# Optimization experiments

Hardware: AMD Instinct MI355X
Metric: run time of the kernel (lower is better)

The kernel has to match this reference:

```python
import jax, jax.numpy as jnp
import numpy as np

NEG = -10000.0
SLOPE = 0.2


def setup_inputs() -> dict:
    key = jax.random.key(0)
    k1, k2, k3, k4, k5 = jax.random.split(key, 5)
    B, N, F_in, F_out = 8, 2048, 512, 512
    text = jax.random.normal(k1, (B, N, F_in), dtype=jnp.float32)
    adj = jax.random.randint(k2, (B, N, N), 0, 2, dtype=jnp.int32)
    sc = 1.0 / np.sqrt(F_in)
    W = jax.random.normal(k3, (F_in, F_out), dtype=jnp.float32) * sc
    b = jnp.zeros((F_out,), dtype=jnp.float32)
    a_src = jax.random.normal(k4, (F_out,), dtype=jnp.float32) * sc
    a_dst = jax.random.normal(k5, (F_out,), dtype=jnp.float32) * sc
    return {"text": text, "adj": adj, "W": W, "b": b, "a_src": a_src, "a_dst": a_dst}


def reference(text, adj, W, b, a_src, a_dst):
    # hidden: [B, N, F_out]
    hidden = jnp.einsum("bnf,fo->bno", text, W) + b
    s = jnp.einsum("bno,o->bn", hidden, a_src)  # src score per node
    d = jnp.einsum("bno,o->bn", hidden, a_dst)  # dst score per node
    scores = s[:, :, None] + d[:, None, :]      # [B, N, N]
    scores = jnp.where(scores >= 0, scores, SLOPE * scores)  # LeakyReLU
    # faithful to original: masked_fill where adj.bool() is True
    scores = jnp.where(adj.astype(bool), NEG, scores)
    attn = jax.nn.softmax(scores, axis=-1)
    return jnp.einsum("bnm,bmo->bno", attn, hidden)
```

## Files before the change

### kernel.cpp

```cpp
#include <hip/hip_runtime.h>
#include <stdint.h>

#define NB 8
#define NN 2048
#define NF 512
#define TOTN (NB * NN)

typedef unsigned short u16;
typedef short bf16x8 __attribute__((ext_vector_type(8)));
typedef float f32x4 __attribute__((ext_vector_type(4)));

__device__ __forceinline__ u16 f2bf(float x) {
  unsigned u = __float_as_uint(x);
  unsigned r = 0x7FFFu + ((u >> 16) & 1u);
  return (u16)((u + r) >> 16);
}

__device__ __forceinline__ void gl2lds16(const void* g, void* l) {
  __builtin_amdgcn_global_load_lds((const __attribute__((address_space(1))) void*)g,
                                   (__attribute__((address_space(3))) void*)l,
                                   16, 0, 0);
}


__global__ __launch_bounds__(256) void conv_kernel(
    const float* __restrict__ text, const float* __restrict__ W,
    u16* __restrict__ text_bf, u16* __restrict__ Wt) {
  int blk = blockIdx.x;
  if (blk < 8192) {
    int idx = blk * 256 + threadIdx.x;
    float4 v = ((const float4*)text)[idx];
    ushort4 o;
    o.x = f2bf(v.x); o.y = f2bf(v.y); o.z = f2bf(v.z); o.w = f2bf(v.w);
    ((ushort4*)text_bf)[idx] = o;
  } else {
    int t = (blk - 8192) * 256 + threadIdx.x;
    int o = t >> 9, f = t & 511;
    Wt[o * NF + f] = f2bf(W[f * NF + o]);
  }
}

__global__ __launch_bounds__(256) void pack_kernel(
    const int* __restrict__ adj, uint32_t* __restrict__ bm) {
  int bid = blockIdx.x;
  int z = bid & 7, idx = bid >> 3;
  int gid = z * 131072 + idx * 256 + threadIdx.x;
  const int4* p = (const int4*)(adj + (size_t)gid * 32);
  uint32_t bits = 0;
#pragma unroll
  for (int c = 0; c < 8; ++c) {
    int4 a = p[c];
    bits |= (uint32_t)(a.x != 0) << (c * 4 + 0);
    bits |= (uint32_t)(a.y != 0) << (c * 4 + 1);
    bits |= (uint32_t)(a.z != 0) << (c * 4 + 2);
    bits |= (uint32_t)(a.w != 0) << (c * 4 + 3);
  }
  bm[gid] = bits;
}

__global__ __launch_bounds__(256) void gemm1_kernel(
    const u16* __restrict__ A,
    const u16* __restrict__ Bt,
    const float* __restrict__ bias, const float* __restrict__ a_src,
    const float* __restrict__ a_dst, u16* __restrict__ Bg,
    float* __restrict__ s, float* __restrict__ d) {
  __shared__ u16 Alds[128 * 32];
  __shared__ u16 Blds[128 * 32];

  const int bid = blockIdx.x;
  const int zx = bid & 7, u = (bid >> 3) & 15, bm_ = bid >> 7;
  const int bn = zx * 16 + u;
  const int t = threadIdx.x, wave = t >> 6, lane = t & 63;
  const int wm = (wave >> 1) * 64, wn = (wave & 1) * 64;

  f32x4 acc[4][4];
#pragma unroll
  for (int i = 0; i < 4; ++i)
#pragma unroll
    for (int j = 0; j < 4; ++j) acc[i][j] = (f32x4){0.f, 0.f, 0.f, 0.f};

  const int rowA0 = bm_ * 128, rowB0 = bn * 128;
  const int srow = (lane >> 2);
  const int scol = (lane & 3) * 8;

  for (int kt = 0; kt < NF; kt += 32) {
#pragma unroll
    for (int q = 0; q < 2; ++q) {
      int r = wave * 32 + q * 16;
      gl2lds16(A + (size_t)(rowA0 + r + srow) * NF + (kt + scol), &Alds[r * 32]);
    }
#pragma unroll
    for (int q = 0; q < 2; ++q) {
      int r = wave * 32 + q * 16;
      gl2lds16(Bt + (size_t)(rowB0 + r + srow) * NF + (kt + scol), &Blds[r * 32]);
    }
    __syncthreads();

    const int fr = lane & 15;
    const int k0 = (lane >> 4) * 8;
    bf16x8 af[4], bfr[4];
#pragma unroll
    for (int i = 0; i < 4; ++i)
      af[i] = *(const bf16x8*)&Alds[(wm + i * 16 + fr) * 32 + k0];
#pragma unroll
    for (int j = 0; j < 4; ++j)
      bfr[j] = *(const bf16x8*)&Blds[(wn + j * 16 + fr) * 32 + k0];
#pragma unroll
    for (int i = 0; i < 4; ++i)
#pragma unroll
      for (int j = 0; j < 4; ++j)
        acc[i][j] = __builtin_amdgcn_mfma_f32_16x16x32_bf16(af[i], bfr[j],
                                                            acc[i][j], 0, 0, 0);
    __syncthreads();
  }

  const int quad = lane >> 4, ln16 = lane & 15;
  float sa[4] = {0.f, 0.f, 0.f, 0.f}, da[4] = {0.f, 0.f, 0.f, 0.f};
#pragma unroll
  for (int i = 0; i < 4; ++i) {
    int m0 = bm_ * 128 + wm + i * 16 + quad * 4;
#pragma unroll
    for (int r = 0; r < 4; ++r) {
      int m = m0 + r;
      float bv = bias[m];
      float asv = a_src[m], adv = a_dst[m];
      int oc = m >> 4, oln = m & 15;
#pragma unroll
      for (int j = 0; j < 4; ++j) {
        int n = bn * 128 + wn + j * 16 + ln16;
        float h = acc[i][j][r] + bv;
        int zz = n >> 11, nz = n & 2047;
        int kc = nz >> 5, kq = (nz >> 3) & 3, ke = nz & 7;
        size_t off = ((size_t)zz << 20) + (((size_t)kc * 32 + oc) << 9) +
                     ((kq * 16 + oln) << 3) + ke;
        Bg[off] = f2bf(h);
        sa[j] = fmaf(h, asv, sa[j]);
        da[j] = fmaf(h, adv, da[j]);
      }
    }
  }
#pragma unroll
  for (int j = 0; j < 4; ++j) {
    float v = sa[j] + __shfl_xor(sa[j], 16, 64);
    v += __shfl_xor(v, 32, 64);
    float w2 = da[j] + __shfl_xor(da[j], 16, 64);
    w2 += __shfl_xor(w2, 32, 64);
    if (quad == 0) {
      int n = bn * 128 + wn + j * 16 + ln16;
      atomicAdd(&s[n], v);
      atomicAdd(&d[n], w2);
    }
  }
}

__global__ __launch_bounds__(512, 2) void fused_attn_kernel(
    const uint32_t* __restrict__ bm, const float* __restrict__ s,
    const float* __restrict__ d, const u16* __restrict__ Bg,
    float* __restrict__ out) {
  __shared__ u16 Plds[2][4096];
  __shared__ float lpart[512];
  __shared__ float linv_lds[64];

  const int bid = blockIdx.x;
  const int z = bid & 7;
  const int i0 = (bid >> 3) * 64;
  const int t = threadIdx.x, wave = t >> 6, lane = t & 63;
  const int quad = lane >> 4, ln16 = lane & 15;

  const int pr = t >> 3;
  const int ko = (t & 7) * 8;
  const float si = s[z * NN + i0 + pr];
  const uint32_t* bmrow = bm + (size_t)(z * NN + i0 + pr) * 64;
  const float* db = d + z * NN;

  const u16* BgZ = Bg + ((size_t)z << 20);

  f32x4 acc[4][4];
#pragma unroll
  for (int i = 0; i < 4; ++i)
#pragma unroll
    for (int j = 0; j < 4; ++j) acc[i][j] = (f32x4){0.f, 0.f, 0.f, 0.f};

  uint32_t bw = bmrow[ko >> 5];
  float4 dv0 = *(const float4*)&db[ko];
  float4 dv1 = *(const float4*)&db[ko + 4];

  const int prc = pr & 15, pch = pr >> 4;
  const int ph = ko >> 5, pq = (ko >> 3) & 3;
  const int pwoff = ph * 2048 + pch * 512 +
                    (prc * 4 + (pq ^ ((prc >> 1) & 3))) * 8;
  const int fslot = ln16 * 4 + (quad ^ ((ln16 >> 1) & 3));

  float lsum = 0.f;
  int par = 0;

  for (int kt = 0; kt < NN; kt += 64, par ^= 1) {
    uint32_t bits8 = (bw >> (ko & 31)) & 0xFFu;
    float dva[8];
    *(float4*)&dva[0] = dv0;
    *(float4*)&dva[4] = dv1;
    u16 pk[8];
#pragma unroll
    for (int e = 0; e < 8; ++e) {
      float x = si + dva[e];
      float xm = fmaxf(x, 0.2f * x);
      float p = ((bits8 >> e) & 1u) ? 0.f : __expf(xm);
      lsum += p;
      pk[e] = f2bf(p);
    }
    *(int4*)((u16*)Plds + par * 4096 + pwoff) = *(int4*)pk;

    __syncthreads();

    const int kc0 = kt >> 5;
    bf16x8 bfr[2][4];
#pragma unroll
    for (int h = 0; h < 2; ++h)
#pragma unroll
      for (int j = 0; j < 4; ++j)
        bfr[h][j] = *(const bf16x8*)&BgZ[(((size_t)(kc0 + h) * 32 +
                                           (wave * 4 + j)) << 9) + lane * 8];

    if (kt + 64 < NN) {
      bw = bmrow[((kt + 64) >> 5) + (ko >> 5)];
      dv0 = *(const float4*)&db[kt + 64 + ko];
      dv1 = *(const float4*)&db[kt + 64 + ko + 4];
    }

    bf16x8 af[2][4];
#pragma unroll
    for (int h = 0; h < 2; ++h)
#pragma unroll
      for (int i = 0; i < 4; ++i)
        af[h][i] = *(const bf16x8*)((const u16*)Plds + par * 4096 + h * 2048 +
                                    i * 512 + fslot * 8);
#pragma unroll
    for (int h = 0; h < 2; ++h)
#pragma unroll
      for (int i = 0; i < 4; ++i)
#pragma unroll
        for (int j = 0; j < 4; ++j)
          acc[i][j] = __builtin_amdgcn_mfma_f32_16x16x32_bf16(af[h][i],
                                                              bfr[h][j],
                                                              acc[i][j], 0, 0, 0);
  }

  lpart[pr * 8 + (t & 7)] = lsum;
  __syncthreads();
  if (t < 64) {
    const float* lp = &lpart[t * 8];
    float tot = ((lp[0] + lp[1]) + (lp[2] + lp[3])) +
                ((lp[4] + lp[5]) + (lp[6] + lp[7]));
    linv_lds[t] = 1.0f / tot;
  }
  __syncthreads();

#pragma unroll
  for (int i = 0; i < 4; ++i) {
#pragma unroll
    for (int r = 0; r < 4; ++r) {
      int m = i * 16 + quad * 4 + r;
      float sc = linv_lds[m];
      float* ob = out + ((size_t)(z * NN) + i0 + m) * NF + wave * 64;
#pragma unroll
      for (int j = 0; j < 4; ++j) ob[j * 16 + ln16] = acc[i][j][r] * sc;
    }
  }
}

extern "C" void kernel_launch(void* const* d_in, const int* in_sizes, int n_in,
                              void* d_out, int out_size, void* d_ws,
                              size_t ws_size, hipStream_t stream) {
  const float* text  = (const float*)d_in[0];
  const int*   adj   = (const int*)d_in[1];
  const float* W     = (const float*)d_in[2];
  const float* bias  = (const float*)d_in[3];
  const float* a_src = (const float*)d_in[4];
  const float* a_dst = (const float*)d_in[5];
  float* out = (float*)d_out;

  char* ws = (char*)d_ws;
  u16*      text_bf = (u16*)(ws + 0);
  u16*      Wt      = (u16*)(ws + 16777216);
  u16*      Bg      = (u16*)(ws + 17301504);
  float*    s       = (float*)(ws + 34078720);
  float*    d       = (float*)(ws + 34144256);
  uint32_t* bmask   = (uint32_t*)(ws + 34209792);

  hipMemsetAsync(s, 0, 131072, stream);

  conv_kernel<<<9216, 256, 0, stream>>>(text, W, text_bf, Wt);
  pack_kernel<<<4096, 256, 0, stream>>>(adj, bmask);

  gemm1_kernel<<<512, 256, 0, stream>>>(Wt, text_bf, bias, a_src, a_dst, Bg, s, d);

  fused_attn_kernel<<<256, 512, 0, stream>>>(bmask, s, d, Bg, out);
}
```

Baseline: 303.5 us.

## Compute softmax probabilities in registers as MFMA A-fragments, drop LDS staging

The attention kernel now has each wave build its P fragments directly in registers in the MFMA A-operand layout, removing the shared-memory P buffer and its per-iteration barrier. To match, the adjacency bitmask is stored column-major and the hidden matrix layout is re-tiled into 128-wide output-feature slabs. Blocks now tile 256 rows by 128 output features with 256 threads, so the exp work is repeated across the four feature slabs. P also uses cheaper round-half-up bf16 conversion. The cost is 4x redundant exp/mask computation, more accumulator registers (4x8 tiles), and uncoalesced 4-byte bitmask reads.

```diff
diff --git a/kernel.cpp b/kernel.cpp
--- a/kernel.cpp
+++ b/kernel.cpp
@@ -14,6 +14,10 @@
   unsigned u = __float_as_uint(x);
   unsigned r = 0x7FFFu + ((u >> 16) & 1u);
   return (u16)((u + r) >> 16);
+}
+
+__device__ __forceinline__ float felem(float4 q, int e) {
+  return (e == 0) ? q.x : (e == 1) ? q.y : (e == 2) ? q.z : q.w;
 }
 
 __device__ __forceinline__ void gl2lds16(const void* g, void* l) {
@@ -41,11 +45,12 @@
 }
 
 __global__ __launch_bounds__(256) void pack_kernel(
-    const int* __restrict__ adj, uint32_t* __restrict__ bm) {
+    const int* __restrict__ adj, uint32_t* __restrict__ bmT) {
   int bid = blockIdx.x;
   int z = bid & 7, idx = bid >> 3;
-  int gid = z * 131072 + idx * 256 + threadIdx.x;
-  const int4* p = (const int4*)(adj + (size_t)gid * 32);
+  int widx = idx * 256 + threadIdx.x;
+  int row = widx >> 6, col = widx & 63;
+  const int4* p = (const int4*)(adj + ((size_t)z * 131072 + widx) * 32);
   uint32_t bits = 0;
 #pragma unroll
   for (int c = 0; c < 8; ++c) {
@@ -55,7 +60,7 @@
     bits |= (uint32_t)(a.z != 0) << (c * 4 + 2);
     bits |= (uint32_t)(a.w != 0) << (c * 4 + 3);
   }
-  bm[gid] = bits;
+  bmT[z * 131072 + col * 2048 + row] = bits;
 }
 
 __global__ __launch_bounds__(256) void gemm1_kernel(
@@ -124,14 +129,14 @@
       int m = m0 + r;
       float bv = bias[m];
       float asv = a_src[m], adv = a_dst[m];
-      int oc = m >> 4, oln = m & 15;
+      int otp = m >> 7, jf = (m >> 4) & 7, oln = m & 15;
 #pragma unroll
       for (int j = 0; j < 4; ++j) {
         int n = bn * 128 + wn + j * 16 + ln16;
         float h = acc[i][j][r] + bv;
         int zz = n >> 11, nz = n & 2047;
         int kc = nz >> 5, kq = (nz >> 3) & 3, ke = nz & 7;
-        size_t off = ((size_t)zz << 20) + (((size_t)kc * 32 + oc) << 9) +
+        size_t off = (((size_t)zz * 4 + otp) << 18) + (kc << 12) + (jf << 9) +
                      ((kq * 16 + oln) << 3) + ke;
         Bg[off] = f2bf(h);
         sa[j] = fmaf(h, asv, sa[j]);
@@ -153,117 +158,126 @@
   }
 }
 
-__global__ __launch_bounds__(512, 2) void fused_attn_kernel(
-    const uint32_t* __restrict__ bm, const float* __restrict__ s,
+__global__ __launch_bounds__(256, 1) void fused_attn_kernel(
+    const uint32_t* __restrict__ bmT, const float* __restrict__ s,
     const float* __restrict__ d, const u16* __restrict__ Bg,
     float* __restrict__ out) {
-  __shared__ u16 Plds[2][4096];
-  __shared__ float lpart[512];
-  __shared__ float linv_lds[64];
+  __shared__ float linv_lds[4][64];
 
   const int bid = blockIdx.x;
   const int z = bid & 7;
-  const int i0 = (bid >> 3) * 64;
+  const int rest = bid >> 3;
+  const int it = rest & 7, ot = rest >> 3;
   const int t = threadIdx.x, wave = t >> 6, lane = t & 63;
   const int quad = lane >> 4, ln16 = lane & 15;
-
-  const int pr = t >> 3;
-  const int ko = (t & 7) * 8;
-  const float si = s[z * NN + i0 + pr];
-  const uint32_t* bmrow = bm + (size_t)(z * NN + i0 + pr) * 64;
-  const float* db = d + z * NN;
-
-  const u16* BgZ = Bg + ((size_t)z << 20);
-
-  f32x4 acc[4][4];
-#pragma unroll
-  for (int i = 0; i < 4; ++i)
-#pragma unroll
-    for (int j = 0; j < 4; ++j) acc[i][j] = (f32x4){0.f, 0.f, 0.f, 0.f};
-
-  uint32_t bw = bmrow[ko >> 5];
-  float4 dv0 = *(const float4*)&db[ko];
-  float4 dv1 = *(const float4*)&db[ko + 4];
-
-  const int prc = pr & 15, pch = pr >> 4;
-  const int ph = ko >> 5, pq = (ko >> 3) & 3;
-  const int pwoff = ph * 2048 + pch * 512 +
-                    (prc * 4 + (pq ^ ((prc >> 1) & 3))) * 8;
-  const int fslot = ln16 * 4 + (quad ^ ((ln16 >> 1) & 3));
-
-  float lsum = 0.f;
-  int par = 0;
-
-  for (int kt = 0; kt < NN; kt += 64, par ^= 1) {
-    uint32_t bits8 = (bw >> (ko & 31)) & 0xFFu;
-    float dva[8];
-    *(float4*)&dva[0] = dv0;
-    *(float4*)&dva[4] = dv1;
-    u16 pk[8];
-#pragma unroll
-    for (int e = 0; e < 8; ++e) {
-      float x = si + dva[e];
-      float xm = fmaxf(x, 0.2f * x);
-      float p = ((bits8 >> e) & 1u) ? 0.f : __expf(xm);
-      lsum += p;
-      pk[e] = f2bf(p);
-    }
-    *(int4*)((u16*)Plds + par * 4096 + pwoff) = *(int4*)pk;
-
-    __syncthreads();
-
+  const int i0w = it * 256 + wave * 64;
+
+  const float* sz = s + z * NN;
+  const float* dz = d + z * NN;
+  const uint32_t* bmz = bmT + z * 131072;
+  const u16* BgW = Bg + (((size_t)z * 4 + ot) << 18);
+
+  float si[4];
+  int rowv[4];
+#pragma unroll
+  for (int f = 0; f < 4; ++f) {
+    rowv[f] = i0w + f * 16 + ln16;
+    si[f] = sz[rowv[f]];
+  }
+
+  f32x4 acc[4][8];
+#pragma unroll
+  for (int f = 0; f < 4; ++f)
+#pragma unroll
+    for (int j = 0; j < 8; ++j) acc[f][j] = (f32x4){0.f, 0.f, 0.f, 0.f};
+
+  float lsum[4] = {0.f, 0.f, 0.f, 0.f};
+
+  uint32_t wcur[4][2];
+  float4 dcur[4];
+#pragma unroll
+  for (int f = 0; f < 4; ++f) {
+    wcur[f][0] = bmz[0 * 2048 + rowv[f]];
+    wcur[f][1] = bmz[1 * 2048 + rowv[f]];
+  }
+#pragma unroll
+  for (int h = 0; h < 2; ++h)
+#pragma unroll
+    for (int c = 0; c < 2; ++c)
+      dcur[h * 2 + c] = *(const float4*)&dz[h * 32 + quad * 8 + c * 4];
+
+  for (int kt = 0; kt < NN; kt += 64) {
     const int kc0 = kt >> 5;
-    bf16x8 bfr[2][4];
+
+    bf16x8 bfr[2][8];
 #pragma unroll
     for (int h = 0; h < 2; ++h)
 #pragma unroll
-      for (int j = 0; j < 4; ++j)
-        bfr[h][j] = *(const bf16x8*)&BgZ[(((size_t)(kc0 + h) * 32 +
-                                           (wave * 4 + j)) << 9) + lane * 8];
+      for (int j = 0; j < 8; ++j)
+        bfr[h][j] = *(const bf16x8*)&BgW[(size_t)(kc0 + h) * 4096 + j * 512 +
+                                         lane * 8];
+
+    bf16x8 af[2][4];
+#pragma unroll
+    for (int f = 0; f < 4; ++f) {
+#pragma unroll
+      for (int h = 0; h < 2; ++h) {
+        uint32_t bits = wcur[f][h] >> (quad * 8);
+#pragma unroll
+        for (int e = 0; e < 8; ++e) {
+          float dj = felem(dcur[h * 2 + (e >> 2)], e & 3);
+          float x = si[f] + dj;
+          float xm = fmaxf(x, 0.2f * x);
+          float p = ((bits >> e) & 1u) ? 0.f : __expf(xm);
+          lsum[f] += p;
+          af[h][f][e] = (short)((__float_as_uint(p) + 0x8000u) >> 16);
+        }
+      }
+    }
 
     if (kt + 64 < NN) {
-      bw = bmrow[((kt + 64) >> 5) + (ko >> 5)];
-      dv0 = *(const float4*)&db[kt + 64 + ko];
-      dv1 = *(const float4*)&db[kt + 64 + ko + 4];
-    }
-
-    bf16x8 af[2][4];
+      int c0 = (kt + 64) >> 5;
+#pragma unroll
+      for (int f = 0; f < 4; ++f) {
+        wcur[f][0] = bmz[(c0 + 0) * 2048 + rowv[f]];
+        wcur[f][1] = bmz[(c0 + 1) * 2048 + rowv[f]];
+      }
+#pragma unroll
+      for (int h = 0; h < 2; ++h)
+#pragma unroll
+        for (int c = 0; c < 2; ++c)
+          dcur[h * 2 + c] =
+              *(const float4*)&dz[kt + 64 + h * 32 + quad * 8 + c * 4];
+    }
+
 #pragma unroll
     for (int h = 0; h < 2; ++h)
 #pragma unroll
-      for (int i = 0; i < 4; ++i)
-        af[h][i] = *(const bf16x8*)((const u16*)Plds + par * 4096 + h * 2048 +
-                                    i * 512 + fslot * 8);
-#pragma unroll
-    for (int h = 0; h < 2; ++h)
-#pragma unroll
-      for (int i = 0; i < 4; ++i)
-#pragma unroll
-        for (int j = 0; j < 4; ++j)
-          acc[i][j] = __builtin_amdgcn_mfma_f32_16x16x32_bf16(af[h][i],
+      for (int f = 0; f < 4; ++f)
+#pragma unroll
+        for (int j = 0; j < 8; ++j)
+          acc[f][j] = __builtin_amdgcn_mfma_f32_16x16x32_bf16(af[h][f],
                                                               bfr[h][j],
-                                                              acc[i][j], 0, 0, 0);
-  }
-
-  lpart[pr * 8 + (t & 7)] = lsum;
+                                                              acc[f][j], 0, 0, 0);
+  }
+
+#pragma unroll
+  for (int f = 0; f < 4; ++f) {
+    lsum[f] += __shfl_xor(lsum[f], 16, 64);
+    lsum[f] += __shfl_xor(lsum[f], 32, 64);
+    if (quad == 0) linv_lds[wave][f * 16 + ln16] = 1.0f / lsum[f];
+  }
   __syncthreads();
-  if (t < 64) {
-    const float* lp = &lpart[t * 8];
-    float tot = ((lp[0] + lp[1]) + (lp[2] + lp[3])) +
-                ((lp[4] + lp[5]) + (lp[6] + lp[7]));
-    linv_lds[t] = 1.0f / tot;
-  }
-  __syncthreads();
-
-#pragma unroll
-  for (int i = 0; i < 4; ++i) {
+
+#pragma unroll
+  for (int f = 0; f < 4; ++f) {
 #pragma unroll
     for (int r = 0; r < 4; ++r) {
-      int m = i * 16 + quad * 4 + r;
-      float sc = linv_lds[m];
-      float* ob = out + ((size_t)(z * NN) + i0 + m) * NF + wave * 64;
-#pragma unroll
-      for (int j = 0; j < 4; ++j) ob[j * 16 + ln16] = acc[i][j][r] * sc;
+      int m = f * 16 + quad * 4 + r;
+      float sc = linv_lds[wave][m];
+      float* ob = out + ((size_t)(z * NN) + i0w + m) * NF + ot * 128;
+#pragma unroll
+      for (int j = 0; j < 8; ++j) ob[j * 16 + ln16] = acc[f][j][r] * sc;
     }
   }
 }
@@ -285,14 +299,14 @@
   u16*      Bg      = (u16*)(ws + 17301504);
   float*    s       = (float*)(ws + 34078720);
   float*    d       = (float*)(ws + 34144256);
-  uint32_t* bmask   = (uint32_t*)(ws + 34209792);
+  uint32_t* bmT     = (uint32_t*)(ws + 34209792);
 
   hipMemsetAsync(s, 0, 131072, stream);
 
   conv_kernel<<<9216, 256, 0, stream>>>(text, W, text_bf, Wt);
-  pack_kernel<<<4096, 256, 0, stream>>>(adj, bmask);
+  pack_kernel<<<4096, 256, 0, stream>>>(adj, bmT);
 
   gemm1_kernel<<<512, 256, 0, stream>>>(Wt, text_bf, bias, a_src, a_dst, Bg, s, d);
 
-  fused_attn_kernel<<<256, 512, 0, stream>>>(bmask, s, d, Bg, out);
-}
+  fused_attn_kernel<<<256, 256, 0, stream>>>(bmT, s, d, Bg, out);
+}
```

Result: slower. 330.4 us (+8.9%).

## Split attention output columns across blocks and transpose packed adjacency mask

Applied to the files above, without the earlier changes.

The fused attention kernel now runs 512 blocks of 256 threads, with each block covering 64 rows and half of the 512 output features, instead of 256 blocks of 512 threads covering all features. Each thread computes 16 probabilities per tile instead of 8. The packed adjacency bitmask is stored transposed so per-row mask words are read column-major. The intent is more blocks for better CU occupancy and balance, but every probability tile (exp, LeakyReLU, mask) is now computed twice, once per feature half, and pack_kernel writes its mask words in a strided pattern.

```diff
diff --git a/kernel.cpp b/kernel.cpp
--- a/kernel.cpp
+++ b/kernel.cpp
@@ -14,6 +14,10 @@
   unsigned u = __float_as_uint(x);
   unsigned r = 0x7FFFu + ((u >> 16) & 1u);
   return (u16)((u + r) >> 16);
+}
+
+__device__ __forceinline__ float felem(float4 q, int e) {
+  return (e == 0) ? q.x : (e == 1) ? q.y : (e == 2) ? q.z : q.w;
 }
 
 __device__ __forceinline__ void gl2lds16(const void* g, void* l) {
@@ -41,11 +45,12 @@
 }
 
 __global__ __launch_bounds__(256) void pack_kernel(
-    const int* __restrict__ adj, uint32_t* __restrict__ bm) {
+    const int* __restrict__ adj, uint32_t* __restrict__ bmT) {
   int bid = blockIdx.x;
   int z = bid & 7, idx = bid >> 3;
-  int gid = z * 131072 + idx * 256 + threadIdx.x;
-  const int4* p = (const int4*)(adj + (size_t)gid * 32);
+  int widx = idx * 256 + threadIdx.x;
+  int row = widx >> 6, col = widx & 63;
+  const int4* p = (const int4*)(adj + ((size_t)z * 131072 + widx) * 32);
   uint32_t bits = 0;
 #pragma unroll
   for (int c = 0; c < 8; ++c) {
@@ -55,7 +60,7 @@
     bits |= (uint32_t)(a.z != 0) << (c * 4 + 2);
     bits |= (uint32_t)(a.w != 0) << (c * 4 + 3);
   }
-  bm[gid] = bits;
+  bmT[z * 131072 + col * 2048 + row] = bits;
 }
 
 __global__ __launch_bounds__(256) void gemm1_kernel(
@@ -153,117 +158,127 @@
   }
 }
 
-__global__ __launch_bounds__(512, 2) void fused_attn_kernel(
-    const uint32_t* __restrict__ bm, const float* __restrict__ s,
+__global__ __launch_bounds__(256, 2) void fused_attn_kernel(
+    const uint32_t* __restrict__ bmT, const float* __restrict__ s,
     const float* __restrict__ d, const u16* __restrict__ Bg,
     float* __restrict__ out) {
   __shared__ u16 Plds[2][4096];
-  __shared__ float lpart[512];
+  __shared__ float lpart[256];
   __shared__ float linv_lds[64];
 
   const int bid = blockIdx.x;
   const int z = bid & 7;
-  const int i0 = (bid >> 3) * 64;
+  const int rest = bid >> 3;
+  const int it = rest & 31, ot = rest >> 5;
+  const int i0 = it * 64;
   const int t = threadIdx.x, wave = t >> 6, lane = t & 63;
   const int quad = lane >> 4, ln16 = lane & 15;
 
-  const int pr = t >> 3;
-  const int ko = (t & 7) * 8;
-  const float si = s[z * NN + i0 + pr];
-  const uint32_t* bmrow = bm + (size_t)(z * NN + i0 + pr) * 64;
-  const float* db = d + z * NN;
+  const int pr = t >> 2;
+  const int ks = (t & 3) * 16;
+  const int prow = i0 + pr;
+  const float si = s[z * NN + prow];
+  const uint32_t* bmz = bmT + z * 131072;
+  const float* dz = d + z * NN;
 
   const u16* BgZ = Bg + ((size_t)z << 20);
+  const int ofb = ot * 16 + wave * 4;
 
   f32x4 acc[4][4];
 #pragma unroll
-  for (int i = 0; i < 4; ++i)
-#pragma unroll
-    for (int j = 0; j < 4; ++j) acc[i][j] = (f32x4){0.f, 0.f, 0.f, 0.f};
-
-  uint32_t bw = bmrow[ko >> 5];
-  float4 dv0 = *(const float4*)&db[ko];
-  float4 dv1 = *(const float4*)&db[ko + 4];
+  for (int f = 0; f < 4; ++f)
+#pragma unroll
+    for (int j = 0; j < 4; ++j) acc[f][j] = (f32x4){0.f, 0.f, 0.f, 0.f};
 
   const int prc = pr & 15, pch = pr >> 4;
-  const int ph = ko >> 5, pq = (ko >> 3) & 3;
-  const int pwoff = ph * 2048 + pch * 512 +
-                    (prc * 4 + (pq ^ ((prc >> 1) & 3))) * 8;
+  const int ph = ks >> 5, pq = (ks >> 3) & 3;
+  const int pwoff0 = ph * 2048 + pch * 512 +
+                     (prc * 4 + (pq ^ ((prc >> 1) & 3))) * 8;
+  const int pwoff1 = ph * 2048 + pch * 512 +
+                     (prc * 4 + ((pq + 1) ^ ((prc >> 1) & 3))) * 8;
   const int fslot = ln16 * 4 + (quad ^ ((ln16 >> 1) & 3));
+
+  uint32_t wcur = bmz[(ks >> 5) * 2048 + prow];
+  float4 dcur[4];
+#pragma unroll
+  for (int g = 0; g < 4; ++g) dcur[g] = *(const float4*)&dz[ks + g * 4];
 
   float lsum = 0.f;
   int par = 0;
 
   for (int kt = 0; kt < NN; kt += 64, par ^= 1) {
-    uint32_t bits8 = (bw >> (ko & 31)) & 0xFFu;
-    float dva[8];
-    *(float4*)&dva[0] = dv0;
-    *(float4*)&dva[4] = dv1;
-    u16 pk[8];
-#pragma unroll
-    for (int e = 0; e < 8; ++e) {
-      float x = si + dva[e];
-      float xm = fmaxf(x, 0.2f * x);
-      float p = ((bits8 >> e) & 1u) ? 0.f : __expf(xm);
-      lsum += p;
-      pk[e] = f2bf(p);
-    }
-    *(int4*)((u16*)Plds + par * 4096 + pwoff) = *(int4*)pk;
+    const int kc0 = kt >> 5;
+
+    uint32_t bits16 = wcur >> (ks & 16);
+    u16 pk[16];
+#pragma unroll
+    for (int g = 0; g < 4; ++g) {
+      float4 dq = dcur[g];
+#pragma unroll
+      for (int e = 0; e < 4; ++e) {
+        float x = si + felem(dq, e);
+        float xm = fmaxf(x, 0.2f * x);
+        float p = ((bits16 >> (g * 4 + e)) & 1u) ? 0.f : __expf(xm);
+        lsum += p;
+        pk[g * 4 + e] = f2bf(p);
+      }
+    }
+    u16* Pbuf = &Plds[par][0];
+    *(int4*)(Pbuf + pwoff0) = *(int4*)&pk[0];
+    *(int4*)(Pbuf + pwoff1) = *(int4*)&pk[8];
 
     __syncthreads();
 
-    const int kc0 = kt >> 5;
     bf16x8 bfr[2][4];
 #pragma unroll
     for (int h = 0; h < 2; ++h)
 #pragma unroll
       for (int j = 0; j < 4; ++j)
-        bfr[h][j] = *(const bf16x8*)&BgZ[(((size_t)(kc0 + h) * 32 +
-                                           (wave * 4 + j)) << 9) + lane * 8];
+        bfr[h][j] = *(const bf16x8*)&BgZ[(((size_t)(kc0 + h) * 32) + ofb + j) *
+                                             512 + lane * 8];
+
+    bf16x8 af[2][4];
+#pragma unroll
+    for (int h = 0; h < 2; ++h)
+#pragma unroll
+      for (int f = 0; f < 4; ++f)
+        af[h][f] = *(const bf16x8*)(Pbuf + h * 2048 + f * 512 + fslot * 8);
 
     if (kt + 64 < NN) {
-      bw = bmrow[((kt + 64) >> 5) + (ko >> 5)];
-      dv0 = *(const float4*)&db[kt + 64 + ko];
-      dv1 = *(const float4*)&db[kt + 64 + ko + 4];
-    }
-
-    bf16x8 af[2][4];
+      wcur = bmz[(((kt + 64) >> 5) + (ks >> 5)) * 2048 + prow];
+#pragma unroll
+      for (int g = 0; g < 4; ++g)
+        dcur[g] = *(const float4*)&dz[kt + 64 + ks + g * 4];
+    }
+
 #pragma unroll
     for (int h = 0; h < 2; ++h)
 #pragma unroll
-      for (int i = 0; i < 4; ++i)
-        af[h][i] = *(const bf16x8*)((const u16*)Plds + par * 4096 + h * 2048 +
-                                    i * 512 + fslot * 8);
-#pragma unroll
-    for (int h = 0; h < 2; ++h)
-#pragma unroll
-      for (int i = 0; i < 4; ++i)
+      for (int f = 0; f < 4; ++f)
 #pragma unroll
         for (int j = 0; j < 4; ++j)
-          acc[i][j] = __builtin_amdgcn_mfma_f32_16x16x32_bf16(af[h][i],
+          acc[f][j] = __builtin_amdgcn_mfma_f32_16x16x32_bf16(af[h][f],
                                                               bfr[h][j],
-                                                              acc[i][j], 0, 0, 0);
-  }
-
-  lpart[pr * 8 + (t & 7)] = lsum;
+                                                              acc[f][j], 0, 0, 0);
+  }
+
+  lpart[pr * 4 + (t & 3)] = lsum;
   __syncthreads();
   if (t < 64) {
-    const float* lp = &lpart[t * 8];
-    float tot = ((lp[0] + lp[1]) + (lp[2] + lp[3])) +
-                ((lp[4] + lp[5]) + (lp[6] + lp[7]));
-    linv_lds[t] = 1.0f / tot;
+    const float* lp = &lpart[t * 4];
+    linv_lds[t] = 1.0f / ((lp[0] + lp[1]) + (lp[2] + lp[3]));
   }
   __syncthreads();
 
 #pragma unroll
-  for (int i = 0; i < 4; ++i) {
+  for (int f = 0; f < 4; ++f) {
 #pragma unroll
     for (int r = 0; r < 4; ++r) {
-      int m = i * 16 + quad * 4 + r;
+      int m = f * 16 + quad * 4 + r;
       float sc = linv_lds[m];
-      float* ob = out + ((size_t)(z * NN) + i0 + m) * NF + wave * 64;
-#pragma unroll
-      for (int j = 0; j < 4; ++j) ob[j * 16 + ln16] = acc[i][j][r] * sc;
+      float* ob = out + ((size_t)(z * NN) + i0 + m) * NF + ot * 256 + wave * 64;
+#pragma unroll
+      for (int j = 0; j < 4; ++j) ob[j * 16 + ln16] = acc[f][j][r] * sc;
     }
   }
 }
@@ -285,14 +300,14 @@
   u16*      Bg      = (u16*)(ws + 17301504);
   float*    s       = (float*)(ws + 34078720);
   float*    d       = (float*)(ws + 34144256);
-  uint32_t* bmask   = (uint32_t*)(ws + 34209792);
+  uint32_t* bmT     = (uint32_t*)(ws + 34209792);
 
   hipMemsetAsync(s, 0, 131072, stream);
 
   conv_kernel<<<9216, 256, 0, stream>>>(text, W, text_bf, Wt);
-  pack_kernel<<<4096, 256, 0, stream>>>(adj, bmask);
+  pack_kernel<<<4096, 256, 0, stream>>>(adj, bmT);
 
   gemm1_kernel<<<512, 256, 0, stream>>>(Wt, text_bf, bias, a_src, a_dst, Bg, s, d);
 
-  fused_attn_kernel<<<256, 512, 0, stream>>>(bmask, s, d, Bg, out);
-}
+  fused_attn_kernel<<<512, 256, 0, stream>>>(bmT, s, d, Bg, out);
+}
```

New measurement: 310.3 us. 2.2% more time.
